# Performance work log

Hardware: AMD Instinct MI355X
Metric: run time of the kernel (lower is better)

The kernel has to match this reference:

```python
import jax, jax.numpy as jnp
import numpy as np


def _hard_sigmoid(x):
    # Keras ConvLSTM2D default recurrent_activation
    return jnp.clip(0.2 * x + 0.5, 0.0, 1.0)


def _conv(x, w):
    # NHWC input, HWIO kernel, SAME padding, stride 1
    return jax.lax.conv_general_dilated(
        x, w, (1, 1), 'SAME', dimension_numbers=('NHWC', 'HWIO', 'NHWC'))


def _convlstm(seq, h, c, k, rk, b):
    # seq: [B, T, H, W, Cin]; h, c: [B, H, W, F]
    # k: [kh, kw, Cin, 4F], rk: [kh, kw, F, 4F], b: [4F]
    def step(carry, x):
        h, c = carry
        z = _conv(x, k) + _conv(h, rk) + b  # [B,H,W,4F]
        zi, zf, zc, zo = jnp.split(z, 4, axis=-1)
        i = _hard_sigmoid(zi)
        f = _hard_sigmoid(zf)
        o = _hard_sigmoid(zo)
        c = f * c + i * jnp.tanh(zc)
        h = o * jnp.tanh(c)
        return (h, c), None
    (h, c), _ = jax.lax.scan(step, (h, c), jnp.swapaxes(seq, 0, 1))
    return h, c


def setup_inputs() -> dict:
    key = jax.random.key(0)
    ks = jax.random.split(key, 14)
    B, T, H, W, Cin, F, K = 32, 1, 64, 64, 1, 64, 3
    s = 0.05
    inp = {
        'input_': jax.random.normal(ks[0], (B, T, H, W, Cin), jnp.float32),
        'h0': jax.random.normal(ks[1], (B, H, W, F), jnp.float32) * s,
        'c0': jax.random.normal(ks[2], (B, H, W, F), jnp.float32) * s,
        'h1': jax.random.normal(ks[3], (B, H, W, F), jnp.float32) * s,
        'c1': jax.random.normal(ks[4], (B, H, W, F), jnp.float32) * s,
        'k0': jax.random.normal(ks[5], (K, K, Cin, 4 * F), jnp.float32) * s,
        'rk0': jax.random.normal(ks[6], (K, K, F, 4 * F), jnp.float32) * s,
        'b0': jnp.zeros((4 * F,), jnp.float32),
        'k1': jax.random.normal(ks[7], (K, K, F, 4 * F), jnp.float32) * s,
        'rk1': jax.random.normal(ks[8], (K, K, F, 4 * F), jnp.float32) * s,
        'b1': jnp.zeros((4 * F,), jnp.float32),
        'cw': jax.random.normal(ks[9], (1, 1, F, 1), jnp.float32) * s,
        'cb': jnp.zeros((1,), jnp.float32),
    }
    return inp


def reference(input_, h0, c0, h1, c1, k0, rk0, b0, k1, rk1, b1, cw, cb):
    # Layer 0 consumes the input frame sequence (T=1)
    h0n, c0n = _convlstm(input_, h0, c0, k0, rk0, b0)
    # Layer 1 consumes layer-0's last hidden state as its (length-1) input
    h1n, c1n = _convlstm(h0n[:, None], h1, c1, k1, rk1, b1)
    frames = _conv(h1n, cw) + cb  # 1x1 conv head -> [B,H,W,1]
    return frames, h0n, c0n, h1n, c1n
```

## Files before the change

### kernel.cpp

```cpp
#include <hip/hip_runtime.h>
#include <hip/hip_bf16.h>

typedef short s16;
typedef __attribute__((ext_vector_type(8))) short bf16x8;
typedef __attribute__((ext_vector_type(4))) float f32x4;

__device__ __forceinline__ s16 f2bf(float f) {
  unsigned u = __builtin_bit_cast(unsigned, f);
  unsigned r = (u + 0x7FFFu + ((u >> 16) & 1u)) >> 16;
  return (s16)r;
}

__device__ __forceinline__ float hsig(float x) {
  return fminf(fmaxf(0.2f * x + 0.5f, 0.0f), 1.0f);
}

#define PXS 66
#define ROWSZ (PXS * 64)
#define ASZ4 (4 * ROWSZ)
#define ASZ6 (6 * ROWSZ)

__global__ void wprep_kernel(const float* __restrict__ rk0, const float* __restrict__ k1,
                             const float* __restrict__ rk1, const float* __restrict__ k0,
                             s16* __restrict__ w0q, s16* __restrict__ w1q,
                             s16* __restrict__ w2q, s16* __restrict__ k0t) {
  int idx = blockIdx.x * 256 + threadIdx.x;
  const int n1 = 18 * 8192;
  if (idx < 3 * n1) {
    int which = idx / n1;
    int i = idx - which * n1;
    int e    = i & 7;
    int lane = (i >> 3) & 63;
    int g    = (i >> 9) & 3;
    int j    = (i >> 11) & 3;
    int k    = (i >> 13) & 1;
    int tap  = i >> 14;
    int l15 = lane & 15, l4 = lane >> 4;
    int ic = k * 32 + l4 * 8 + e;
    int oc = j * 64 + g * 16 + l15;
    const float* src = (which == 0) ? rk0 : (which == 1) ? k1 : rk1;
    s16* dst = (which == 0) ? w0q : (which == 1) ? w1q : w2q;
    dst[i] = f2bf(src[(tap * 64 + ic) * 256 + oc]);
  } else if (idx < 3 * n1 + 8192) {
    int r = idx - 3 * n1;
    int kk = r & 31;
    int oc = r >> 5;
    k0t[r] = (kk < 9) ? f2bf(k0[kk * 256 + oc]) : (s16)0;
  }
}

template <bool F32>
__device__ __forceinline__ bf16x8 load_conv8(const void* src, long off) {
  if constexpr (F32) {
    const float* p = (const float*)src + off;
    float4 v0 = *reinterpret_cast<const float4*>(p);
    float4 v1 = *reinterpret_cast<const float4*>(p + 4);
    bf16x8 r;
    r[0] = f2bf(v0.x); r[1] = f2bf(v0.y); r[2] = f2bf(v0.z); r[3] = f2bf(v0.w);
    r[4] = f2bf(v1.x); r[5] = f2bf(v1.y); r[6] = f2bf(v1.z); r[7] = f2bf(v1.w);
    return r;
  } else {
    return *reinterpret_cast<const bf16x8*>((const s16*)src + off);
  }
}

template <bool F32, int ROWS, int NT>
__device__ __forceinline__ void stageA(s16* a_lds, const void* src, int b, int y0, int tid) {
  #pragma unroll
  for (int i = 0; i < ROWS * 512 / NT; ++i) {
    int c   = tid + i * NT;
    int row = c >> 9;
    int px  = (c >> 3) & 63;
    int cb  = c & 7;
    int y   = y0 - 1 + row;
    int xp  = px + 1;
    bf16x8 v = {};
    if ((unsigned)y < 64u)
      v = load_conv8<F32>(src, ((long)(b * 64 + y) * 64 + px) * 64 + cb * 8);
    *reinterpret_cast<bf16x8*>(a_lds + (row * PXS + xp) * 64 + ((cb ^ (xp & 7)) * 8)) = v;
  }
  if (tid < ROWS * 16) {
    int row = tid >> 4;
    int xp  = ((tid >> 3) & 1) ? 65 : 0;
    int cb  = tid & 7;
    bf16x8 z = {};
    *reinterpret_cast<bf16x8*>(a_lds + (row * PXS + xp) * 64 + cb * 8) = z;
  }
}

__global__ __launch_bounds__(1024, 1) void cell0_kernel(
    const float* __restrict__ h0,
    const s16* __restrict__ w0,
    const float* __restrict__ xin,
    const s16* __restrict__ k0t,
    const float* __restrict__ bias,
    const float* __restrict__ c_old,
    float* __restrict__ h_out,
    float* __restrict__ c_out,
    s16* __restrict__ hb_out)
{
  __shared__ __align__(16) s16 a_lds[ASZ6];
  __shared__ __align__(16) s16 w_lds[3][8192];
  __shared__ float x_lds[384];

  const int tid = threadIdx.x;
  const int b  = blockIdx.x >> 4;
  const int y0 = (blockIdx.x & 15) << 2;

  const int wave = tid >> 6;
  const int lane = tid & 63;
  const int g    = wave & 3;
  const int mh   = wave >> 2;
  const int l15  = lane & 15;
  const int l4   = lane >> 4;

  constexpr int NST = 18;

  auto issueW = [&](int u) {
    int v = (u >= NST) ? u - NST : u;
    const s16* wt = w0 + v * 8192;
    char* base = (char*)(&w_lds[0][0]) + (v % 3) * 16384 + (tid >> 6) * 1024;
    __builtin_amdgcn_global_load_lds(
        (const __attribute__((address_space(1))) void*)(wt + tid * 8),
        (__attribute__((address_space(3))) void*)base, 16, 0, 0);
  };
  auto readWf = [&](bf16x8 (&wf)[4], int slot) {
    const s16* wb = &w_lds[slot][0] + g * 512 + lane * 8;
    #pragma unroll
    for (int j = 0; j < 4; ++j)
      wf[j] = *reinterpret_cast<const bf16x8*>(wb + j * 2048);
  };

  f32x4 acc[4][4] = {};

  auto doStage = [&](const bf16x8 (&wf)[4], int u) {
    int tap = u >> 1, kk = u & 1;
    int dy = tap / 3, dx = tap - dy * 3;
    const char* sb = (const char*)a_lds + (mh + dy) * (ROWSZ * 2);
    bf16x8 af[4];
    #pragma unroll
    for (int m = 0; m < 4; ++m) {
      int xq   = m * 16 + l15 + dx;
      int boff = xq * 128 + ((((kk << 2) | l4) ^ (xq & 7)) << 4);
      af[m] = *reinterpret_cast<const bf16x8*>(sb + boff);
    }
    __builtin_amdgcn_s_setprio(1);
    #pragma unroll
    for (int m = 0; m < 4; ++m) {
      #pragma unroll
      for (int j = 0; j < 4; ++j)
        acc[m][j] = __builtin_amdgcn_mfma_f32_16x16x32_bf16(af[m], wf[j], acc[m][j], 0, 0, 0);
    }
    __builtin_amdgcn_s_setprio(0);
  };

  issueW(0);
  issueW(1);
  stageA<true, 6, 1024>(a_lds, h0, b, y0, tid);
  if (tid < 384) {
    int row = tid >> 6, px = tid & 63;
    int y = y0 - 1 + row;
    x_lds[tid] = ((unsigned)y < 64u) ? xin[(b * 64 + y) * 64 + px] : 0.0f;
  }
  __syncthreads();

  {
    bf16x8 bx[4];
    #pragma unroll
    for (int j = 0; j < 4; ++j) {
      int oc = j * 64 + g * 16 + l15;
      bx[j] = *reinterpret_cast<const bf16x8*>(k0t + oc * 32 + l4 * 8);
    }
    #pragma unroll
    for (int m = 0; m < 4; ++m) {
      int px = m * 16 + l15;
      bf16x8 ax = {};
      #pragma unroll
      for (int e = 0; e < 8; ++e) {
        int t = l4 * 8 + e;
        if (t < 9) {
          int dyt = t / 3, dxt = t - dyt * 3;
          int xx = px + dxt - 1;
          float xv = ((unsigned)xx < 64u) ? x_lds[(mh + dyt) * 64 + xx] : 0.0f;
          ax[e] = f2bf(xv);
        }
      }
      #pragma unroll
      for (int j = 0; j < 4; ++j)
        acc[m][j] = __builtin_amdgcn_mfma_f32_16x16x32_bf16(ax, bx[j], acc[m][j], 0, 0, 0);
    }
  }

  bf16x8 wf[4];
  #pragma unroll
  for (int u = 0; u < NST; ++u) {
    asm volatile("s_waitcnt vmcnt(1)" ::: "memory");
    __builtin_amdgcn_s_barrier();
    __builtin_amdgcn_sched_barrier(0);
    issueW(u + 2);
    readWf(wf, u % 3);
    doStage(wf, u);
  }

  float bi[4];
  #pragma unroll
  for (int j = 0; j < 4; ++j) bi[j] = bias[j * 64 + g * 16 + l15];
  const int pix_base = b * 4096 + y0 * 64;
  const int f = g * 16 + l15;
  #pragma unroll
  for (int m = 0; m < 4; ++m) {
    #pragma unroll
    for (int r = 0; r < 4; ++r) {
      int pl = mh * 64 + m * 16 + l4 * 4 + r;
      int off = (pix_base + pl) * 64 + f;
      float zi = acc[m][0][r] + bi[0];
      float zf = acc[m][1][r] + bi[1];
      float zc = acc[m][2][r] + bi[2];
      float zo = acc[m][3][r] + bi[3];
      float ig = hsig(zi), fg = hsig(zf), og = hsig(zo);
      float cn = fg * c_old[off] + ig * tanhf(zc);
      float hn = og * tanhf(cn);
      c_out[off] = cn;
      h_out[off] = hn;
      hb_out[off] = f2bf(hn);
    }
  }
}

#define ZP 260
__global__ __launch_bounds__(512, 2) void cell1_kernel(
    const s16* __restrict__ src0,
    const float* __restrict__ src1,
    const s16* __restrict__ w0,
    const s16* __restrict__ w1,
    const float* __restrict__ bias,
    const float* __restrict__ c_old,
    float* __restrict__ h_out,
    float* __restrict__ c_out)
{
  __shared__ __align__(16) s16 a_lds[2 * ASZ4];

  const int tid = threadIdx.x;
  const int b  = blockIdx.x >> 5;
  const int y0 = (blockIdx.x & 31) << 1;

  const int wave = tid >> 6;
  const int lane = tid & 63;
  const int j    = wave & 3;
  const int fh   = wave >> 2;
  const int l15  = lane & 15;
  const int l4   = lane >> 4;

  bf16x8 wreg[18][2];
  {
    const s16* wb = w0 + j * 2048 + fh * 1024 + lane * 8;
    #pragma unroll
    for (int u = 0; u < 18; ++u) {
      wreg[u][0] = *reinterpret_cast<const bf16x8*>(wb + u * 8192);
      wreg[u][1] = *reinterpret_cast<const bf16x8*>(wb + u * 8192 + 512);
    }
  }

  stageA<false, 4, 512>(a_lds, src0, b, y0, tid);
  stageA<true, 4, 512>(a_lds + ASZ4, src1, b, y0, tid);
  __syncthreads();

  f32x4 acc[8][2] = {};

  #pragma unroll
  for (int u = 0; u < 18; ++u) {
    int tap = u >> 1, kk = u & 1;
    int dy = tap / 3, dx = tap - dy * 3;
    #pragma unroll
    for (int m = 0; m < 8; ++m) {
      int row  = (m >> 2) + dy;
      int xq   = (m & 3) * 16 + l15 + dx;
      int boff = xq * 128 + ((((kk << 2) | l4) ^ (xq & 7)) << 4);
      bf16x8 a = *reinterpret_cast<const bf16x8*>((const char*)a_lds + row * (ROWSZ * 2) + boff);
      acc[m][0] = __builtin_amdgcn_mfma_f32_16x16x32_bf16(a, wreg[u][0], acc[m][0], 0, 0, 0);
      acc[m][1] = __builtin_amdgcn_mfma_f32_16x16x32_bf16(a, wreg[u][1], acc[m][1], 0, 0, 0);
    }
  }

  {
    const s16* wb = w1 + j * 2048 + fh * 1024 + lane * 8;
    #pragma unroll
    for (int u = 0; u < 18; ++u) {
      wreg[u][0] = *reinterpret_cast<const bf16x8*>(wb + u * 8192);
      wreg[u][1] = *reinterpret_cast<const bf16x8*>(wb + u * 8192 + 512);
    }
  }

  #pragma unroll
  for (int u = 0; u < 18; ++u) {
    int tap = u >> 1, kk = u & 1;
    int dy = tap / 3, dx = tap - dy * 3;
    #pragma unroll
    for (int m = 0; m < 8; ++m) {
      int row  = (m >> 2) + dy;
      int xq   = (m & 3) * 16 + l15 + dx;
      int boff = xq * 128 + ((((kk << 2) | l4) ^ (xq & 7)) << 4);
      bf16x8 a = *reinterpret_cast<const bf16x8*>((const char*)a_lds + ASZ4 * 2 + row * (ROWSZ * 2) + boff);
      acc[m][0] = __builtin_amdgcn_mfma_f32_16x16x32_bf16(a, wreg[u][0], acc[m][0], 0, 0, 0);
      acc[m][1] = __builtin_amdgcn_mfma_f32_16x16x32_bf16(a, wreg[u][1], acc[m][1], 0, 0, 0);
    }
  }

  float* z_lds = (float*)a_lds;
  const int pix_base = b * 4096 + y0 * 64;
  #pragma unroll
  for (int h = 0; h < 2; ++h) {
    __syncthreads();
    #pragma unroll
    for (int mm = 0; mm < 4; ++mm) {
      #pragma unroll
      for (int q = 0; q < 2; ++q) {
        int oc = j * 64 + fh * 32 + q * 16 + l15;
        #pragma unroll
        for (int r = 0; r < 4; ++r) {
          int px = mm * 16 + l4 * 4 + r;
          z_lds[px * ZP + oc] = acc[h * 4 + mm][q][r];
        }
      }
    }
    __syncthreads();
    int px8 = wave * 8 + (lane >> 3);
    int f0  = (lane & 7) * 8;
    const float* zr = z_lds + px8 * ZP;
    int off0 = (pix_base + h * 64 + px8) * 64 + f0;
    #pragma unroll
    for (int half8 = 0; half8 < 2; ++half8) {
      float4 zi4 = *reinterpret_cast<const float4*>(zr + f0 + half8 * 4);
      float4 zf4 = *reinterpret_cast<const float4*>(zr + 64 + f0 + half8 * 4);
      float4 zc4 = *reinterpret_cast<const float4*>(zr + 128 + f0 + half8 * 4);
      float4 zo4 = *reinterpret_cast<const float4*>(zr + 192 + f0 + half8 * 4);
      float4 bi4 = *reinterpret_cast<const float4*>(bias + f0 + half8 * 4);
      float4 bf4 = *reinterpret_cast<const float4*>(bias + 64 + f0 + half8 * 4);
      float4 bc4 = *reinterpret_cast<const float4*>(bias + 128 + f0 + half8 * 4);
      float4 bo4 = *reinterpret_cast<const float4*>(bias + 192 + f0 + half8 * 4);
      float4 co4 = *reinterpret_cast<const float4*>(c_old + off0 + half8 * 4);
      float4 hn4, cn4;
      #pragma unroll
      for (int e = 0; e < 4; ++e) {
        float zi = (&zi4.x)[e] + (&bi4.x)[e];
        float zf = (&zf4.x)[e] + (&bf4.x)[e];
        float zc = (&zc4.x)[e] + (&bc4.x)[e];
        float zo = (&zo4.x)[e] + (&bo4.x)[e];
        float ig = hsig(zi), fg = hsig(zf), og = hsig(zo);
        float cn = fg * (&co4.x)[e] + ig * tanhf(zc);
        (&cn4.x)[e] = cn;
        (&hn4.x)[e] = og * tanhf(cn);
      }
      *reinterpret_cast<float4*>(c_out + off0 + half8 * 4) = cn4;
      *reinterpret_cast<float4*>(h_out + off0 + half8 * 4) = hn4;
    }
  }
}

__global__ void frames_kernel(const float* __restrict__ h, const float* __restrict__ cw,
                              const float* __restrict__ cbp, float* __restrict__ out) {
  int tid = blockIdx.x * 256 + threadIdx.x;
  int p  = tid >> 2;
  int fc = (tid & 3) * 16;
  const float4* hp = reinterpret_cast<const float4*>(h + p * 64 + fc);
  const float4* wp = reinterpret_cast<const float4*>(cw + fc);
  float s = 0.0f;
  #pragma unroll
  for (int i = 0; i < 4; ++i) {
    float4 v = hp[i];
    float4 w = wp[i];
    s += v.x * w.x + v.y * w.y + v.z * w.z + v.w * w.w;
  }
  s += __shfl_xor(s, 1);
  s += __shfl_xor(s, 2);
  if ((tid & 3) == 0) out[p] = s + cbp[0];
}

extern "C" void kernel_launch(void* const* d_in, const int* in_sizes, int n_in,
                              void* d_out, int out_size, void* d_ws, size_t ws_size,
                              hipStream_t stream) {
  const float* x   = (const float*)d_in[0];
  const float* h0  = (const float*)d_in[1];
  const float* c0  = (const float*)d_in[2];
  const float* h1  = (const float*)d_in[3];
  const float* c1  = (const float*)d_in[4];
  const float* k0  = (const float*)d_in[5];
  const float* rk0 = (const float*)d_in[6];
  const float* b0  = (const float*)d_in[7];
  const float* k1  = (const float*)d_in[8];
  const float* rk1 = (const float*)d_in[9];
  const float* b1  = (const float*)d_in[10];
  const float* cw  = (const float*)d_in[11];
  const float* cbp = (const float*)d_in[12];

  float* out    = (float*)d_out;
  float* frames = out;
  float* h0n    = out + 131072;
  float* c0n    = out + 131072 + 8388608;
  float* h1n    = out + 131072 + 2 * 8388608;
  float* c1n    = out + 131072 + 3 * 8388608;

  char* ws = (char*)d_ws;
  const size_t SZ_H = 16777216;
  s16* h0nb = (s16*)(ws + 0 * SZ_H);
  s16* w0q  = (s16*)(ws + 1 * SZ_H);
  s16* w1q  = (s16*)(ws + 1 * SZ_H + 1 * 294912);
  s16* w2q  = (s16*)(ws + 1 * SZ_H + 2 * 294912);
  s16* k0t  = (s16*)(ws + 1 * SZ_H + 3 * 294912);

  wprep_kernel<<<1760, 256, 0, stream>>>(rk0, k1, rk1, k0, w0q, w1q, w2q, k0t);

  cell0_kernel<<<512, 1024, 0, stream>>>(
      h0, w0q, x, k0t, b0, c0, h0n, c0n, h0nb);

  cell1_kernel<<<1024, 512, 0, stream>>>(
      h0nb, h1, w1q, w2q, b1, c1, h1n, c1n);

  frames_kernel<<<2048, 256, 0, stream>>>(h1n, cw, cbp, frames);
}
```

Before: 208.3 us.

## Split cell1 work across 16 waves with per-row tiles and chunked weight loads

The layer-1 cell kernel goes from 512 to 1024 threads per block. Each wave now handles one output row and a quarter of the gate channels, so its accumulators shrink from 8x2 to 4x2 fragments. Weights are loaded one K-half at a time (9x2 fragments instead of 18x2), which lowers register pressure so the kernel can run under launch bounds of 1024 threads with 4 blocks per CU. The cost is more passes over LDS A-tiles and more reloads of weight fragments per wave.

```diff
diff --git a/kernel.cpp b/kernel.cpp
--- a/kernel.cpp
+++ b/kernel.cpp
@@ -228,7 +228,7 @@
 }
 
 #define ZP 260
-__global__ __launch_bounds__(512, 2) void cell1_kernel(
+__global__ __launch_bounds__(1024, 4) void cell1_kernel(
     const s16* __restrict__ src0,
     const float* __restrict__ src1,
     const s16* __restrict__ w0,
@@ -246,114 +246,95 @@
 
   const int wave = tid >> 6;
   const int lane = tid & 63;
-  const int j    = wave & 3;
-  const int fh   = wave >> 2;
+  const int mh   = wave >> 3;
+  const int s8   = wave & 7;
+  const int jj   = s8 >> 1;
+  const int g0   = (s8 & 1) * 2;
   const int l15  = lane & 15;
   const int l4   = lane >> 4;
 
-  bf16x8 wreg[18][2];
-  {
-    const s16* wb = w0 + j * 2048 + fh * 1024 + lane * 8;
-    #pragma unroll
-    for (int u = 0; u < 18; ++u) {
-      wreg[u][0] = *reinterpret_cast<const bf16x8*>(wb + u * 8192);
-      wreg[u][1] = *reinterpret_cast<const bf16x8*>(wb + u * 8192 + 512);
-    }
-  }
-
-  stageA<false, 4, 512>(a_lds, src0, b, y0, tid);
-  stageA<true, 4, 512>(a_lds + ASZ4, src1, b, y0, tid);
+  stageA<false, 4, 1024>(a_lds, src0, b, y0, tid);
+  stageA<true, 4, 1024>(a_lds + ASZ4, src1, b, y0, tid);
   __syncthreads();
 
-  f32x4 acc[8][2] = {};
-
-  #pragma unroll
-  for (int u = 0; u < 18; ++u) {
-    int tap = u >> 1, kk = u & 1;
-    int dy = tap / 3, dx = tap - dy * 3;
-    #pragma unroll
-    for (int m = 0; m < 8; ++m) {
-      int row  = (m >> 2) + dy;
-      int xq   = (m & 3) * 16 + l15 + dx;
-      int boff = xq * 128 + ((((kk << 2) | l4) ^ (xq & 7)) << 4);
-      bf16x8 a = *reinterpret_cast<const bf16x8*>((const char*)a_lds + row * (ROWSZ * 2) + boff);
-      acc[m][0] = __builtin_amdgcn_mfma_f32_16x16x32_bf16(a, wreg[u][0], acc[m][0], 0, 0, 0);
-      acc[m][1] = __builtin_amdgcn_mfma_f32_16x16x32_bf16(a, wreg[u][1], acc[m][1], 0, 0, 0);
-    }
-  }
-
-  {
-    const s16* wb = w1 + j * 2048 + fh * 1024 + lane * 8;
-    #pragma unroll
-    for (int u = 0; u < 18; ++u) {
-      wreg[u][0] = *reinterpret_cast<const bf16x8*>(wb + u * 8192);
-      wreg[u][1] = *reinterpret_cast<const bf16x8*>(wb + u * 8192 + 512);
-    }
-  }
-
-  #pragma unroll
-  for (int u = 0; u < 18; ++u) {
-    int tap = u >> 1, kk = u & 1;
-    int dy = tap / 3, dx = tap - dy * 3;
-    #pragma unroll
-    for (int m = 0; m < 8; ++m) {
-      int row  = (m >> 2) + dy;
-      int xq   = (m & 3) * 16 + l15 + dx;
-      int boff = xq * 128 + ((((kk << 2) | l4) ^ (xq & 7)) << 4);
-      bf16x8 a = *reinterpret_cast<const bf16x8*>((const char*)a_lds + ASZ4 * 2 + row * (ROWSZ * 2) + boff);
-      acc[m][0] = __builtin_amdgcn_mfma_f32_16x16x32_bf16(a, wreg[u][0], acc[m][0], 0, 0, 0);
-      acc[m][1] = __builtin_amdgcn_mfma_f32_16x16x32_bf16(a, wreg[u][1], acc[m][1], 0, 0, 0);
-    }
-  }
+  f32x4 acc[4][2] = {};
+  const int wloff = jj * 2048 + g0 * 512 + lane * 8;
+
+  auto qpass = [&](const s16* wsrc, const char* abase, int kk) {
+    bf16x8 wreg[9][2];
+    #pragma unroll
+    for (int t = 0; t < 9; ++t) {
+      const s16* wp = wsrc + (t * 2 + kk) * 8192 + wloff;
+      wreg[t][0] = *reinterpret_cast<const bf16x8*>(wp);
+      wreg[t][1] = *reinterpret_cast<const bf16x8*>(wp + 512);
+    }
+    #pragma unroll
+    for (int t = 0; t < 9; ++t) {
+      int dy = t / 3, dx = t - dy * 3;
+      const char* sb = abase + (mh + dy) * (ROWSZ * 2);
+      #pragma unroll
+      for (int m = 0; m < 4; ++m) {
+        int xq   = m * 16 + l15 + dx;
+        int boff = xq * 128 + ((((kk << 2) | l4) ^ (xq & 7)) << 4);
+        bf16x8 a = *reinterpret_cast<const bf16x8*>(sb + boff);
+        acc[m][0] = __builtin_amdgcn_mfma_f32_16x16x32_bf16(a, wreg[t][0], acc[m][0], 0, 0, 0);
+        acc[m][1] = __builtin_amdgcn_mfma_f32_16x16x32_bf16(a, wreg[t][1], acc[m][1], 0, 0, 0);
+      }
+    }
+  };
+
+  qpass(w0, (const char*)a_lds, 0);
+  qpass(w0, (const char*)a_lds, 1);
+  qpass(w1, (const char*)a_lds + ASZ4 * 2, 0);
+  qpass(w1, (const char*)a_lds + ASZ4 * 2, 1);
 
   float* z_lds = (float*)a_lds;
   const int pix_base = b * 4096 + y0 * 64;
   #pragma unroll
   for (int h = 0; h < 2; ++h) {
     __syncthreads();
-    #pragma unroll
-    for (int mm = 0; mm < 4; ++mm) {
+    if (mh == h) {
       #pragma unroll
-      for (int q = 0; q < 2; ++q) {
-        int oc = j * 64 + fh * 32 + q * 16 + l15;
+      for (int m = 0; m < 4; ++m) {
         #pragma unroll
-        for (int r = 0; r < 4; ++r) {
-          int px = mm * 16 + l4 * 4 + r;
-          z_lds[px * ZP + oc] = acc[h * 4 + mm][q][r];
+        for (int q = 0; q < 2; ++q) {
+          int oc = jj * 64 + (g0 + q) * 16 + l15;
+          #pragma unroll
+          for (int r = 0; r < 4; ++r) {
+            int px = m * 16 + l4 * 4 + r;
+            z_lds[px * ZP + oc] = acc[m][q][r];
+          }
         }
       }
     }
     __syncthreads();
-    int px8 = wave * 8 + (lane >> 3);
-    int f0  = (lane & 7) * 8;
-    const float* zr = z_lds + px8 * ZP;
-    int off0 = (pix_base + h * 64 + px8) * 64 + f0;
-    #pragma unroll
-    for (int half8 = 0; half8 < 2; ++half8) {
-      float4 zi4 = *reinterpret_cast<const float4*>(zr + f0 + half8 * 4);
-      float4 zf4 = *reinterpret_cast<const float4*>(zr + 64 + f0 + half8 * 4);
-      float4 zc4 = *reinterpret_cast<const float4*>(zr + 128 + f0 + half8 * 4);
-      float4 zo4 = *reinterpret_cast<const float4*>(zr + 192 + f0 + half8 * 4);
-      float4 bi4 = *reinterpret_cast<const float4*>(bias + f0 + half8 * 4);
-      float4 bf4 = *reinterpret_cast<const float4*>(bias + 64 + f0 + half8 * 4);
-      float4 bc4 = *reinterpret_cast<const float4*>(bias + 128 + f0 + half8 * 4);
-      float4 bo4 = *reinterpret_cast<const float4*>(bias + 192 + f0 + half8 * 4);
-      float4 co4 = *reinterpret_cast<const float4*>(c_old + off0 + half8 * 4);
-      float4 hn4, cn4;
-      #pragma unroll
-      for (int e = 0; e < 4; ++e) {
-        float zi = (&zi4.x)[e] + (&bi4.x)[e];
-        float zf = (&zf4.x)[e] + (&bf4.x)[e];
-        float zc = (&zc4.x)[e] + (&bc4.x)[e];
-        float zo = (&zo4.x)[e] + (&bo4.x)[e];
-        float ig = hsig(zi), fg = hsig(zf), og = hsig(zo);
-        float cn = fg * (&co4.x)[e] + ig * tanhf(zc);
-        (&cn4.x)[e] = cn;
-        (&hn4.x)[e] = og * tanhf(cn);
-      }
-      *reinterpret_cast<float4*>(c_out + off0 + half8 * 4) = cn4;
-      *reinterpret_cast<float4*>(h_out + off0 + half8 * 4) = hn4;
-    }
+    int px = tid >> 4;
+    int f4 = (tid & 15) * 4;
+    const float* zr = z_lds + px * ZP;
+    float4 zi4 = *reinterpret_cast<const float4*>(zr + f4);
+    float4 zf4 = *reinterpret_cast<const float4*>(zr + 64 + f4);
+    float4 zc4 = *reinterpret_cast<const float4*>(zr + 128 + f4);
+    float4 zo4 = *reinterpret_cast<const float4*>(zr + 192 + f4);
+    float4 bi4 = *reinterpret_cast<const float4*>(bias + f4);
+    float4 bf4 = *reinterpret_cast<const float4*>(bias + 64 + f4);
+    float4 bc4 = *reinterpret_cast<const float4*>(bias + 128 + f4);
+    float4 bo4 = *reinterpret_cast<const float4*>(bias + 192 + f4);
+    int off0 = (pix_base + h * 64 + px) * 64 + f4;
+    float4 co4 = *reinterpret_cast<const float4*>(c_old + off0);
+    float4 hn4, cn4;
+    #pragma unroll
+    for (int e = 0; e < 4; ++e) {
+      float zi = (&zi4.x)[e] + (&bi4.x)[e];
+      float zf = (&zf4.x)[e] + (&bf4.x)[e];
+      float zc = (&zc4.x)[e] + (&bc4.x)[e];
+      float zo = (&zo4.x)[e] + (&bo4.x)[e];
+      float ig = hsig(zi), fg = hsig(zf), og = hsig(zo);
+      float cn = fg * (&co4.x)[e] + ig * tanhf(zc);
+      (&cn4.x)[e] = cn;
+      (&hn4.x)[e] = og * tanhf(cn);
+    }
+    *reinterpret_cast<float4*>(c_out + off0) = cn4;
+    *reinterpret_cast<float4*>(h_out + off0) = hn4;
   }
 }
 
@@ -413,7 +394,7 @@
   cell0_kernel<<<512, 1024, 0, stream>>>(
       h0, w0q, x, k0t, b0, c0, h0n, c0n, h0nb);
 
-  cell1_kernel<<<1024, 512, 0, stream>>>(
+  cell1_kernel<<<1024, 1024, 0, stream>>>(
       h0nb, h1, w1q, w2q, b1, c1, h1n, c1n);
 
   frames_kernel<<<2048, 256, 0, stream>>>(h1n, cw, cbp, frames);
```

Result: faster. 181.4 us, median of 2 (-12.9%).
